# Optimization experiments

Hardware: AMD Instinct MI355X
Metric: run time of the kernel (lower is better)

## Reference

```python
import jax, jax.numpy as jnp
import numpy as np

N, IN_DIM, OUT_DIM = 8192, 128, 64
ALPHA = 0.2  # LeakyReLU negative slope
NEG_INF = -1e12


def setup_inputs() -> dict:
    key = jax.random.key(0)
    k1, k2, k3, k4 = jax.random.split(key, 4)
    x = jax.random.normal(k1, (N, IN_DIM), dtype=jnp.float32)
    adj = jax.random.randint(k2, (N, N), 0, 2, dtype=jnp.int32)
    W = jax.random.normal(k3, (IN_DIM, OUT_DIM), dtype=jnp.float32) * 0.1
    a = jax.random.normal(k4, (2 * OUT_DIM, 1), dtype=jnp.float32) * 0.1
    return {"x": x, "adj": adj, "W": W, "a": a}


def reference(x, adj, W, a):
    Wh = x @ W                                   # [N, out_dim]
    Wh1 = Wh @ a[:OUT_DIM, :]                    # [N, 1] source scores
    Wh2 = Wh @ a[OUT_DIM:, :]                    # [N, 1] target scores
    e = Wh1 + Wh2.T                              # [N, N] additive attention
    e = jnp.where(e > 0, e, ALPHA * e)           # LeakyReLU
    scores = jnp.where(adj > 0, e, NEG_INF)      # mask non-edges
    attention = jax.nn.softmax(scores, axis=1)   # row-wise softmax
    h_prime = attention @ Wh                     # [N, out_dim]
    return jax.nn.elu(h_prime)
```

## Files before the change

kernel.cpp:

```cpp
#include <hip/hip_runtime.h>


#define N 8192
#define IN_DIM 128
#define OUT_DIM 64
#define ALPHA 0.2f
#define LOG2E 1.44269504088896f
#define JC 16
#define CW (N / JC)
#define TW 128
#define NT (CW / TW)
#define LDP 136

typedef _Float16 half8 __attribute__((ext_vector_type(8)));
typedef _Float16 half4 __attribute__((ext_vector_type(4)));
typedef float f32x4 __attribute__((ext_vector_type(4)));

__global__ __launch_bounds__(64) void wh_kernel(
    const float* __restrict__ x, const float* __restrict__ W,
    const float* __restrict__ a, _Float16* __restrict__ Wh_t,
    float* __restrict__ s1, float* __restrict__ s2,
    float* __restrict__ s2L) {
  __shared__ float xs[IN_DIM];
  const int i = blockIdx.x;
  const int t = threadIdx.x;

  xs[t]      = x[(size_t)i * IN_DIM + t];
  xs[t + 64] = x[(size_t)i * IN_DIM + 64 + t];
  __syncthreads();

  float wh = 0.f;
#pragma unroll
  for (int d = 0; d < IN_DIM; ++d) wh = fmaf(xs[d], W[d * OUT_DIM + t], wh);

  Wh_t[(size_t)t * N + i] = (_Float16)wh;

  float p1 = wh * a[t];
  float p2 = wh * a[64 + t];
#pragma unroll
  for (int off = 32; off; off >>= 1) {
    p1 += __shfl_down(p1, off);
    p2 += __shfl_down(p2, off);
  }
  if (t == 0) {
    s1[i] = p1;
    s2[i] = p2;
    s2L[i] = p2 * LOG2E;
  }
}

__global__ __launch_bounds__(256) void max_kernel(
    const float* __restrict__ s1, const float* __restrict__ s2,
    float* __restrict__ Mout) {
  __shared__ float red[8];
  const int t = threadIdx.x;
  float m1 = -1e30f, m2 = -1e30f;
  for (int idx = t; idx < N; idx += 256) {
    m1 = fmaxf(m1, s1[idx]);
    m2 = fmaxf(m2, s2[idx]);
  }
#pragma unroll
  for (int off = 32; off; off >>= 1) {
    m1 = fmaxf(m1, __shfl_down(m1, off));
    m2 = fmaxf(m2, __shfl_down(m2, off));
  }
  if ((t & 63) == 0) {
    red[t >> 6] = m1;
    red[4 + (t >> 6)] = m2;
  }
  __syncthreads();
  if (t == 0) {
    m1 = fmaxf(fmaxf(red[0], red[1]), fmaxf(red[2], red[3]));
    m2 = fmaxf(fmaxf(red[4], red[5]), fmaxf(red[6], red[7]));
    float e = m1 + m2;
    Mout[0] = e > 0.f ? e : ALPHA * e;
  }
}

__global__ __launch_bounds__(256, 8) void attn_kernel(
    const int* __restrict__ adj, const _Float16* __restrict__ Wh_t,
    const float* __restrict__ s1, const float* __restrict__ s2L,
    const float* __restrict__ Mptr, float* __restrict__ accp,
    float* __restrict__ lp) {
  __shared__ __align__(16) _Float16 Ps[4 * 16 * LDP];

  const int t = threadIdx.x;
  const int w = t >> 6;
  const int lane = t & 63;
  const int q = lane >> 4;
  const int r16 = lane & 15;
  const int half_ = lane >> 5;
  const int l32 = lane & 31;
  const int i0 = blockIdx.x * 64 + w * 16;
  const int c = blockIdx.y;
  const int jb = c * CW;

  const float ML = Mptr[0] * LOG2E;

  float s1L[8];
#pragma unroll
  for (int it = 0; it < 8; ++it)
    s1L[it] = s1[i0 + 2 * it + half_] * LOG2E;

  half8 bones;
#pragma unroll
  for (int e = 0; e < 8; ++e) bones[e] = (r16 == 0) ? (_Float16)1.0f : (_Float16)0.0f;

  f32x4 acc[5] = {{0.f, 0.f, 0.f, 0.f}, {0.f, 0.f, 0.f, 0.f},
                  {0.f, 0.f, 0.f, 0.f}, {0.f, 0.f, 0.f, 0.f},
                  {0.f, 0.f, 0.f, 0.f}};

  _Float16* Pw = Ps + w * 16 * LDP;
  const _Float16* ldA = Pw + r16 * LDP + q * 8;
  _Float16* stP = Pw + half_ * LDP + l32 * 4;

  for (int jt = 0; jt < NT; ++jt) {
    const int j0 = jb + jt * TW;

    const float4 sv = *(const float4*)(s2L + j0 + l32 * 4);
    const int* ap = adj + (size_t)(i0 + half_) * N + j0 + l32 * 4;

#pragma unroll
    for (int it = 0; it < 8; ++it) {
      const int4 av = *(const int4*)(ap + (size_t)it * (2 * N));
      const float s1v = s1L[it];
      float p0, p1, p2, p3, tt, uu;
      tt = s1v + sv.x; uu = fmaxf(tt, ALPHA * tt); p0 = exp2f(uu - ML);
      tt = s1v + sv.y; uu = fmaxf(tt, ALPHA * tt); p1 = exp2f(uu - ML);
      tt = s1v + sv.z; uu = fmaxf(tt, ALPHA * tt); p2 = exp2f(uu - ML);
      tt = s1v + sv.w; uu = fmaxf(tt, ALPHA * tt); p3 = exp2f(uu - ML);
      half4 hv;
      hv[0] = (_Float16)(av.x != 0 ? p0 : 0.f);
      hv[1] = (_Float16)(av.y != 0 ? p1 : 0.f);
      hv[2] = (_Float16)(av.z != 0 ? p2 : 0.f);
      hv[3] = (_Float16)(av.w != 0 ? p3 : 0.f);
      *(half4*)(stP + it * (2 * LDP)) = hv;
    }

#pragma unroll
    for (int ks = 0; ks < 4; ++ks) {
      const half8 aF = *(const half8*)(ldA + ks * 32);
      const int kcol = j0 + ks * 32 + q * 8;
#pragma unroll
      for (int fg = 0; fg < 4; ++fg) {
        const half8 bf =
            *(const half8*)(Wh_t + (size_t)(fg * 16 + r16) * N + kcol);
        acc[fg] =
            __builtin_amdgcn_mfma_f32_16x16x32_f16(aF, bf, acc[fg], 0, 0, 0);
      }
      acc[4] =
          __builtin_amdgcn_mfma_f32_16x16x32_f16(aF, bones, acc[4], 0, 0, 0);
    }
  }

#pragma unroll
  for (int fg = 0; fg < 4; ++fg) {
#pragma unroll
    for (int r = 0; r < 4; ++r) {
      accp[((size_t)c * N + i0 + q * 4 + r) * OUT_DIM + fg * 16 + r16] =
          acc[fg][r];
    }
  }
  if (r16 == 0) {
#pragma unroll
    for (int r = 0; r < 4; ++r) lp[(size_t)c * N + i0 + q * 4 + r] = acc[4][r];
  }
}

__global__ __launch_bounds__(256) void reduce_kernel(
    const float* __restrict__ accp, const float* __restrict__ lp,
    float* __restrict__ out) {
  const int tid = blockIdx.x * 256 + threadIdx.x;
  const int i = tid >> 6;
  float s = 0.f, l = 0.f;
#pragma unroll
  for (int c = 0; c < JC; ++c) s += accp[(size_t)c * N * OUT_DIM + tid];
#pragma unroll
  for (int c = 0; c < JC; ++c) l += lp[(size_t)c * N + i];
  float v = s / l;
  out[tid] = v > 0.f ? v : expm1f(v);
}

extern "C" void kernel_launch(void* const* d_in, const int* in_sizes, int n_in,
                              void* d_out, int out_size, void* d_ws,
                              size_t ws_size, hipStream_t stream) {
  const float* x = (const float*)d_in[0];
  const int* adj = (const int*)d_in[1];
  const float* W = (const float*)d_in[2];
  const float* a = (const float*)d_in[3];
  float* out = (float*)d_out;

  char* ws = (char*)d_ws;
  _Float16* Wh_t = (_Float16*)ws;
  float* s1 = (float*)(ws + (1u << 20));
  float* s2 = s1 + N;
  float* s2L = s2 + N;
  float* M = s2L + N;
  float* accp = (float*)(ws + (2u << 20));
  float* lp = accp + (size_t)JC * N * OUT_DIM;

  wh_kernel<<<N, 64, 0, stream>>>(x, W, a, Wh_t, s1, s2, s2L);
  max_kernel<<<1, 256, 0, stream>>>(s1, s2, M);
  attn_kernel<<<dim3(N / 64, JC), 256, 0, stream>>>(adj, Wh_t, s1, s2L, M,
                                                    accp, lp);
  reduce_kernel<<<N * OUT_DIM / 256, 256, 0, stream>>>(accp, lp, out);
}
```

Before: 449.3 us.

## Split fused attention into a probability kernel and a separate fp16 MFMA GEMM

Un-fuses the attention kernel. A streaming elementwise kernel now computes masked exp2 probabilities for the full N×N matrix into an fp16 workspace buffer, and a separate MFMA GEMM reads that buffer with fewer K-splits (8 instead of 16). The aim is to decouple the exp/mask work from the matrix-core loop and drop the shared-memory staging and its latency stalls. In exchange it adds a 128 MB intermediate that is written and read back through global memory. Scores are now pre-scaled by log2(e) in wh_kernel, and the max is computed on those scaled values.

After: 482.7 us. 7.4% more time.

```diff
diff --git a/kernel.cpp b/kernel.cpp
--- a/kernel.cpp
+++ b/kernel.cpp
@@ -6,11 +6,7 @@
 #define OUT_DIM 64
 #define ALPHA 0.2f
 #define LOG2E 1.44269504088896f
-#define JC 16
-#define CW (N / JC)
-#define TW 128
-#define NT (CW / TW)
-#define LDP 136
+#define KC 8
 
 typedef _Float16 half8 __attribute__((ext_vector_type(8)));
 typedef _Float16 half4 __attribute__((ext_vector_type(4)));
@@ -19,8 +15,7 @@
 __global__ __launch_bounds__(64) void wh_kernel(
     const float* __restrict__ x, const float* __restrict__ W,
     const float* __restrict__ a, _Float16* __restrict__ Wh_t,
-    float* __restrict__ s1, float* __restrict__ s2,
-    float* __restrict__ s2L) {
+    float* __restrict__ s1L, float* __restrict__ s2L) {
   __shared__ float xs[IN_DIM];
   const int i = blockIdx.x;
   const int t = threadIdx.x;
@@ -43,21 +38,20 @@
     p2 += __shfl_down(p2, off);
   }
   if (t == 0) {
-    s1[i] = p1;
-    s2[i] = p2;
+    s1L[i] = p1 * LOG2E;
     s2L[i] = p2 * LOG2E;
   }
 }
 
 __global__ __launch_bounds__(256) void max_kernel(
-    const float* __restrict__ s1, const float* __restrict__ s2,
+    const float* __restrict__ s1L, const float* __restrict__ s2L,
     float* __restrict__ Mout) {
   __shared__ float red[8];
   const int t = threadIdx.x;
   float m1 = -1e30f, m2 = -1e30f;
   for (int idx = t; idx < N; idx += 256) {
-    m1 = fmaxf(m1, s1[idx]);
-    m2 = fmaxf(m2, s2[idx]);
+    m1 = fmaxf(m1, s1L[idx]);
+    m2 = fmaxf(m2, s2L[idx]);
   }
 #pragma unroll
   for (int off = 32; off; off >>= 1) {
@@ -73,84 +67,73 @@
     m1 = fmaxf(fmaxf(red[0], red[1]), fmaxf(red[2], red[3]));
     m2 = fmaxf(fmaxf(red[4], red[5]), fmaxf(red[6], red[7]));
     float e = m1 + m2;
-    Mout[0] = e > 0.f ? e : ALPHA * e;
+    Mout[0] = fmaxf(e, ALPHA * e);
   }
 }
 
-__global__ __launch_bounds__(256, 8) void attn_kernel(
-    const int* __restrict__ adj, const _Float16* __restrict__ Wh_t,
-    const float* __restrict__ s1, const float* __restrict__ s2L,
-    const float* __restrict__ Mptr, float* __restrict__ accp,
-    float* __restrict__ lp) {
-  __shared__ __align__(16) _Float16 Ps[4 * 16 * LDP];
+__global__ __launch_bounds__(256) void p_kernel(
+    const int* __restrict__ adj, const float* __restrict__ s1L,
+    const float* __restrict__ s2L, const float* __restrict__ Mptr,
+    _Float16* __restrict__ P) {
+  const size_t e0 = ((size_t)blockIdx.x * 256 + threadIdx.x) * 8;
+  const int i = (int)(e0 >> 13);
+  const int j = (int)(e0 & 8191);
+  const float ML = Mptr[0];
+  const float s1v = s1L[i];
 
+  const int4 a0 = *(const int4*)(adj + e0);
+  const int4 a1 = *(const int4*)(adj + e0 + 4);
+  const float4 sa = *(const float4*)(s2L + j);
+  const float4 sb = *(const float4*)(s2L + j + 4);
+
+  const int av[8] = {a0.x, a0.y, a0.z, a0.w, a1.x, a1.y, a1.z, a1.w};
+  const float sv[8] = {sa.x, sa.y, sa.z, sa.w, sb.x, sb.y, sb.z, sb.w};
+  half8 hv;
+#pragma unroll
+  for (int c = 0; c < 8; ++c) {
+    const float tt = s1v + sv[c];
+    const float uu = fmaxf(tt, ALPHA * tt);
+    const float pv = exp2f(uu - ML);
+    hv[c] = (_Float16)(av[c] != 0 ? pv : 0.f);
+  }
+  *(half8*)(P + e0) = hv;
+}
+
+__global__ __launch_bounds__(256, 4) void gemm_kernel(
+    const _Float16* __restrict__ P, const _Float16* __restrict__ Wh_t,
+    float* __restrict__ accp, float* __restrict__ lp) {
   const int t = threadIdx.x;
   const int w = t >> 6;
   const int lane = t & 63;
   const int q = lane >> 4;
   const int r16 = lane & 15;
-  const int half_ = lane >> 5;
-  const int l32 = lane & 31;
   const int i0 = blockIdx.x * 64 + w * 16;
   const int c = blockIdx.y;
-  const int jb = c * CW;
-
-  const float ML = Mptr[0] * LOG2E;
-
-  float s1L[8];
-#pragma unroll
-  for (int it = 0; it < 8; ++it)
-    s1L[it] = s1[i0 + 2 * it + half_] * LOG2E;
+  const int kb = c * (N / KC);
 
   half8 bones;
 #pragma unroll
-  for (int e = 0; e < 8; ++e) bones[e] = (r16 == 0) ? (_Float16)1.0f : (_Float16)0.0f;
+  for (int e = 0; e < 8; ++e)
+    bones[e] = (r16 == 0) ? (_Float16)1.0f : (_Float16)0.0f;
 
   f32x4 acc[5] = {{0.f, 0.f, 0.f, 0.f}, {0.f, 0.f, 0.f, 0.f},
                   {0.f, 0.f, 0.f, 0.f}, {0.f, 0.f, 0.f, 0.f},
                   {0.f, 0.f, 0.f, 0.f}};
 
-  _Float16* Pw = Ps + w * 16 * LDP;
-  const _Float16* ldA = Pw + r16 * LDP + q * 8;
-  _Float16* stP = Pw + half_ * LDP + l32 * 4;
+  const _Float16* pA = P + (size_t)(i0 + r16) * N + kb + q * 8;
+  const _Float16* pB = Wh_t + (size_t)r16 * N + kb + q * 8;
 
-  for (int jt = 0; jt < NT; ++jt) {
-    const int j0 = jb + jt * TW;
-
-    const float4 sv = *(const float4*)(s2L + j0 + l32 * 4);
-    const int* ap = adj + (size_t)(i0 + half_) * N + j0 + l32 * 4;
-
+#pragma unroll 4
+  for (int ks = 0; ks < (N / KC) / 32; ++ks) {
+    const half8 aF = *(const half8*)(pA + ks * 32);
 #pragma unroll
-    for (int it = 0; it < 8; ++it) {
-      const int4 av = *(const int4*)(ap + (size_t)it * (2 * N));
-      const float s1v = s1L[it];
-      float p0, p1, p2, p3, tt, uu;
-      tt = s1v + sv.x; uu = fmaxf(tt, ALPHA * tt); p0 = exp2f(uu - ML);
-      tt = s1v + sv.y; uu = fmaxf(tt, ALPHA * tt); p1 = exp2f(uu - ML);
-      tt = s1v + sv.z; uu = fmaxf(tt, ALPHA * tt); p2 = exp2f(uu - ML);
-      tt = s1v + sv.w; uu = fmaxf(tt, ALPHA * tt); p3 = exp2f(uu - ML);
-      half4 hv;
-      hv[0] = (_Float16)(av.x != 0 ? p0 : 0.f);
-      hv[1] = (_Float16)(av.y != 0 ? p1 : 0.f);
-      hv[2] = (_Float16)(av.z != 0 ? p2 : 0.f);
-      hv[3] = (_Float16)(av.w != 0 ? p3 : 0.f);
-      *(half4*)(stP + it * (2 * LDP)) = hv;
+    for (int fg = 0; fg < 4; ++fg) {
+      const half8 bf = *(const half8*)(pB + (size_t)fg * 16 * N + ks * 32);
+      acc[fg] =
+          __builtin_amdgcn_mfma_f32_16x16x32_f16(aF, bf, acc[fg], 0, 0, 0);
     }
-
-#pragma unroll
-    for (int ks = 0; ks < 4; ++ks) {
-      const half8 aF = *(const half8*)(ldA + ks * 32);
-      const int kcol = j0 + ks * 32 + q * 8;
-#pragma unroll
-      for (int fg = 0; fg < 4; ++fg) {
-        const half8 bf =
-            *(const half8*)(Wh_t + (size_t)(fg * 16 + r16) * N + kcol);
-        acc[fg] =
-            __builtin_amdgcn_mfma_f32_16x16x32_f16(aF, bf, acc[fg], 0, 0, 0);
-      }
-      acc[4] =
-          __builtin_amdgcn_mfma_f32_16x16x32_f16(aF, bones, acc[4], 0, 0, 0);
-    }
+    acc[4] =
+        __builtin_amdgcn_mfma_f32_16x16x32_f16(aF, bones, acc[4], 0, 0, 0);
   }
 
 #pragma unroll
@@ -174,9 +157,9 @@
   const int i = tid >> 6;
   float s = 0.f, l = 0.f;
 #pragma unroll
-  for (int c = 0; c < JC; ++c) s += accp[(size_t)c * N * OUT_DIM + tid];
+  for (int c = 0; c < KC; ++c) s += accp[(size_t)c * N * OUT_DIM + tid];
 #pragma unroll
-  for (int c = 0; c < JC; ++c) l += lp[(size_t)c * N + i];
+  for (int c = 0; c < KC; ++c) l += lp[(size_t)c * N + i];
   float v = s / l;
   out[tid] = v > 0.f ? v : expm1f(v);
 }
@@ -192,16 +175,17 @@
 
   char* ws = (char*)d_ws;
   _Float16* Wh_t = (_Float16*)ws;
-  float* s1 = (float*)(ws + (1u << 20));
-  float* s2 = s1 + N;
-  float* s2L = s2 + N;
+  float* s1L = (float*)(ws + (1u << 20));
+  float* s2L = s1L + N;
   float* M = s2L + N;
-  float* accp = (float*)(ws + (2u << 20));
-  float* lp = accp + (size_t)JC * N * OUT_DIM;
+  _Float16* P = (_Float16*)(ws + (2u << 20));
+  float* accp = (float*)(ws + (132u << 20));
+  float* lp = accp + (size_t)KC * N * OUT_DIM;
 
-  wh_kernel<<<N, 64, 0, stream>>>(x, W, a, Wh_t, s1, s2, s2L);
-  max_kernel<<<1, 256, 0, stream>>>(s1, s2, M);
-  attn_kernel<<<dim3(N / 64, JC), 256, 0, stream>>>(adj, Wh_t, s1, s2L, M,
-                                                    accp, lp);
+  wh_kernel<<<N, 64, 0, stream>>>(x, W, a, Wh_t, s1L, s2L);
+  max_kernel<<<1, 256, 0, stream>>>(s1L, s2L, M);
+  p_kernel<<<(int)((size_t)N * N / 8 / 256), 256, 0, stream>>>(adj, s1L, s2L,
+                                                               M, P);
+  gemm_kernel<<<dim3(N / 64, KC), 256, 0, stream>>>(P, Wh_t, accp, lp);
   reduce_kernel<<<N * OUT_DIM / 256, 256, 0, stream>>>(accp, lp, out);
 }
```

## Prefetch adjacency tiles, pre-pack Wh into MFMA fragments, halve column chunks

Applied to the files above, without the earlier changes.

The attention kernel now loads the next tile's adjacency ints into registers while it computes the current tile, so global load latency overlaps with exp and MFMA work. A new pack kernel lays Wh out in MFMA B-fragment order, which makes each B load one contiguous per-lane read instead of a strided gather. The column split drops from 16 to 8 chunks, which shrinks the partial sums and the reduce traffic but leaves fewer blocks. Occupancy drops to 4 blocks per SM because of the extra registers, and block rows are traversed in reverse. The softmax shift is folded into a multiplier c0 = exp2(-M), and s1 is pre-scaled by log2(e).

Result: faster. 407.0 us (-9.4%).

```diff
diff --git a/kernel.cpp b/kernel.cpp
--- a/kernel.cpp
+++ b/kernel.cpp
@@ -6,7 +6,7 @@
 #define OUT_DIM 64
 #define ALPHA 0.2f
 #define LOG2E 1.44269504088896f
-#define JC 16
+#define JC 8
 #define CW (N / JC)
 #define TW 128
 #define NT (CW / TW)
@@ -19,8 +19,7 @@
 __global__ __launch_bounds__(64) void wh_kernel(
     const float* __restrict__ x, const float* __restrict__ W,
     const float* __restrict__ a, _Float16* __restrict__ Wh_t,
-    float* __restrict__ s1, float* __restrict__ s2,
-    float* __restrict__ s2L) {
+    float* __restrict__ s1L, float* __restrict__ s2L) {
   __shared__ float xs[IN_DIM];
   const int i = blockIdx.x;
   const int t = threadIdx.x;
@@ -43,21 +42,20 @@
     p2 += __shfl_down(p2, off);
   }
   if (t == 0) {
-    s1[i] = p1;
-    s2[i] = p2;
+    s1L[i] = p1 * LOG2E;
     s2L[i] = p2 * LOG2E;
   }
 }
 
 __global__ __launch_bounds__(256) void max_kernel(
-    const float* __restrict__ s1, const float* __restrict__ s2,
-    float* __restrict__ Mout) {
+    const float* __restrict__ s1L, const float* __restrict__ s2L,
+    float* __restrict__ c0out) {
   __shared__ float red[8];
   const int t = threadIdx.x;
   float m1 = -1e30f, m2 = -1e30f;
   for (int idx = t; idx < N; idx += 256) {
-    m1 = fmaxf(m1, s1[idx]);
-    m2 = fmaxf(m2, s2[idx]);
+    m1 = fmaxf(m1, s1L[idx]);
+    m2 = fmaxf(m2, s2L[idx]);
   }
 #pragma unroll
   for (int off = 32; off; off >>= 1) {
@@ -73,14 +71,27 @@
     m1 = fmaxf(fmaxf(red[0], red[1]), fmaxf(red[2], red[3]));
     m2 = fmaxf(fmaxf(red[4], red[5]), fmaxf(red[6], red[7]));
     float e = m1 + m2;
-    Mout[0] = e > 0.f ? e : ALPHA * e;
-  }
-}
-
-__global__ __launch_bounds__(256, 8) void attn_kernel(
-    const int* __restrict__ adj, const _Float16* __restrict__ Wh_t,
-    const float* __restrict__ s1, const float* __restrict__ s2L,
-    const float* __restrict__ Mptr, float* __restrict__ accp,
+    c0out[0] = exp2f(-fmaxf(e, ALPHA * e));
+  }
+}
+
+__global__ __launch_bounds__(256) void bpack_kernel(
+    const _Float16* __restrict__ Wh_t, _Float16* __restrict__ Bpack) {
+  const int kt = blockIdx.x;
+  const int t = threadIdx.x;
+  const int fg = t >> 6;
+  const int lane = t & 63;
+  const int q = (t >> 4) & 3;
+  const int r16 = t & 15;
+  const half8 v =
+      *(const half8*)(Wh_t + (size_t)(fg * 16 + r16) * N + kt * 32 + q * 8);
+  *(half8*)(Bpack + ((size_t)(kt * 4 + fg) * 64 + lane) * 8) = v;
+}
+
+__global__ __launch_bounds__(256, 4) void attn_kernel(
+    const int* __restrict__ adj, const _Float16* __restrict__ Bpack,
+    const float* __restrict__ s1L, const float* __restrict__ s2L,
+    const float* __restrict__ c0p, float* __restrict__ accp,
     float* __restrict__ lp) {
   __shared__ __align__(16) _Float16 Ps[4 * 16 * LDP];
 
@@ -91,66 +102,80 @@
   const int r16 = lane & 15;
   const int half_ = lane >> 5;
   const int l32 = lane & 31;
-  const int i0 = blockIdx.x * 64 + w * 16;
+  const int rb = (int)(gridDim.x - 1 - blockIdx.x);
+  const int i0 = rb * 64 + w * 16;
   const int c = blockIdx.y;
   const int jb = c * CW;
 
-  const float ML = Mptr[0] * LOG2E;
-
-  float s1L[8];
-#pragma unroll
-  for (int it = 0; it < 8; ++it)
-    s1L[it] = s1[i0 + 2 * it + half_] * LOG2E;
+  const float c0 = c0p[0];
+
+  float s1v8[8];
+#pragma unroll
+  for (int it = 0; it < 8; ++it) s1v8[it] = s1L[i0 + 2 * it + half_];
 
   half8 bones;
 #pragma unroll
-  for (int e = 0; e < 8; ++e) bones[e] = (r16 == 0) ? (_Float16)1.0f : (_Float16)0.0f;
+  for (int e = 0; e < 8; ++e)
+    bones[e] = (r16 == 0) ? (_Float16)1.0f : (_Float16)0.0f;
 
   f32x4 acc[5] = {{0.f, 0.f, 0.f, 0.f}, {0.f, 0.f, 0.f, 0.f},
                   {0.f, 0.f, 0.f, 0.f}, {0.f, 0.f, 0.f, 0.f},
                   {0.f, 0.f, 0.f, 0.f}};
 
+  const int* aprow = adj + (size_t)(i0 + half_) * N + jb + l32 * 4;
   _Float16* Pw = Ps + w * 16 * LDP;
   const _Float16* ldA = Pw + r16 * LDP + q * 8;
   _Float16* stP = Pw + half_ * LDP + l32 * 4;
 
+  int4 av[8];
+#pragma unroll
+  for (int it = 0; it < 8; ++it)
+    av[it] = *(const int4*)(aprow + (size_t)(2 * it) * N);
+
   for (int jt = 0; jt < NT; ++jt) {
     const int j0 = jb + jt * TW;
+    const int joff_next = ((jt + 1) & (NT - 1)) * TW;
+
+    int4 nv[8];
+#pragma unroll
+    for (int it = 0; it < 8; ++it)
+      nv[it] = *(const int4*)(aprow + joff_next + (size_t)(2 * it) * N);
 
     const float4 sv = *(const float4*)(s2L + j0 + l32 * 4);
-    const int* ap = adj + (size_t)(i0 + half_) * N + j0 + l32 * 4;
 
 #pragma unroll
     for (int it = 0; it < 8; ++it) {
-      const int4 av = *(const int4*)(ap + (size_t)it * (2 * N));
-      const float s1v = s1L[it];
-      float p0, p1, p2, p3, tt, uu;
-      tt = s1v + sv.x; uu = fmaxf(tt, ALPHA * tt); p0 = exp2f(uu - ML);
-      tt = s1v + sv.y; uu = fmaxf(tt, ALPHA * tt); p1 = exp2f(uu - ML);
-      tt = s1v + sv.z; uu = fmaxf(tt, ALPHA * tt); p2 = exp2f(uu - ML);
-      tt = s1v + sv.w; uu = fmaxf(tt, ALPHA * tt); p3 = exp2f(uu - ML);
+      const float s1v = s1v8[it];
+      float tt, uu;
       half4 hv;
-      hv[0] = (_Float16)(av.x != 0 ? p0 : 0.f);
-      hv[1] = (_Float16)(av.y != 0 ? p1 : 0.f);
-      hv[2] = (_Float16)(av.z != 0 ? p2 : 0.f);
-      hv[3] = (_Float16)(av.w != 0 ? p3 : 0.f);
-      *(half4*)(stP + it * (2 * LDP)) = hv;
+      tt = s1v + sv.x; uu = fmaxf(tt, ALPHA * tt);
+      hv[0] = (_Float16)(av[it].x != 0 ? exp2f(uu) * c0 : 0.f);
+      tt = s1v + sv.y; uu = fmaxf(tt, ALPHA * tt);
+      hv[1] = (_Float16)(av[it].y != 0 ? exp2f(uu) * c0 : 0.f);
+      tt = s1v + sv.z; uu = fmaxf(tt, ALPHA * tt);
+      hv[2] = (_Float16)(av[it].z != 0 ? exp2f(uu) * c0 : 0.f);
+      tt = s1v + sv.w; uu = fmaxf(tt, ALPHA * tt);
+      hv[3] = (_Float16)(av[it].w != 0 ? exp2f(uu) * c0 : 0.f);
+      *(half4*)(stP + (2 * it) * LDP) = hv;
     }
 
+    const int ktb = c * 32 + jt * 4;
 #pragma unroll
     for (int ks = 0; ks < 4; ++ks) {
       const half8 aF = *(const half8*)(ldA + ks * 32);
-      const int kcol = j0 + ks * 32 + q * 8;
+      const _Float16* bp = Bpack + ((size_t)(ktb + ks) * 4 * 64 + lane) * 8;
 #pragma unroll
       for (int fg = 0; fg < 4; ++fg) {
-        const half8 bf =
-            *(const half8*)(Wh_t + (size_t)(fg * 16 + r16) * N + kcol);
+        const half8 bf = *(const half8*)(bp + (size_t)fg * 64 * 8);
         acc[fg] =
             __builtin_amdgcn_mfma_f32_16x16x32_f16(aF, bf, acc[fg], 0, 0, 0);
       }
       acc[4] =
           __builtin_amdgcn_mfma_f32_16x16x32_f16(aF, bones, acc[4], 0, 0, 0);
     }
+
+#pragma unroll
+    for (int it = 0; it < 8; ++it) av[it] = nv[it];
   }
 
 #pragma unroll
@@ -192,16 +217,17 @@
 
   char* ws = (char*)d_ws;
   _Float16* Wh_t = (_Float16*)ws;
-  float* s1 = (float*)(ws + (1u << 20));
-  float* s2 = s1 + N;
-  float* s2L = s2 + N;
-  float* M = s2L + N;
-  float* accp = (float*)(ws + (2u << 20));
+  float* s1L = (float*)(ws + (1u << 20));
+  float* s2L = s1L + N;
+  float* c0 = s2L + N;
+  _Float16* Bpack = (_Float16*)(ws + (2u << 20));
+  float* accp = (float*)(ws + (4u << 20));
   float* lp = accp + (size_t)JC * N * OUT_DIM;
 
-  wh_kernel<<<N, 64, 0, stream>>>(x, W, a, Wh_t, s1, s2, s2L);
-  max_kernel<<<1, 256, 0, stream>>>(s1, s2, M);
-  attn_kernel<<<dim3(N / 64, JC), 256, 0, stream>>>(adj, Wh_t, s1, s2L, M,
+  wh_kernel<<<N, 64, 0, stream>>>(x, W, a, Wh_t, s1L, s2L);
+  max_kernel<<<1, 256, 0, stream>>>(s1L, s2L, c0);
+  bpack_kernel<<<N / 32, 256, 0, stream>>>(Wh_t, Bpack);
+  attn_kernel<<<dim3(N / 64, JC), 256, 0, stream>>>(adj, Bpack, s1L, s2L, c0,
                                                     accp, lp);
   reduce_kernel<<<N * OUT_DIM / 256, 256, 0, stream>>>(accp, lp, out);
 }
```
